# Performance work log

Hardware: AMD Instinct MI355X
Metric: run time of the kernel (lower is better)

Reference implementation:

```python
import jax, jax.numpy as jnp
import numpy as np

HEADS = 16
DIM_HEAD = 64

def setup_inputs() -> dict:
    key = jax.random.key(0)
    ks = jax.random.split(key, 5)
    B, S, D = 2, 2048, 1024
    return {
        "hidden_states": jax.random.normal(ks[0], (B, S, D), dtype=jnp.float32),
        "Wq": jax.random.normal(ks[1], (D, D), dtype=jnp.float32) * (D ** -0.5),
        "Wkv": jax.random.normal(ks[2], (D, D), dtype=jnp.float32) * (D ** -0.5),
        "Wout": jax.random.normal(ks[3], (D, D), dtype=jnp.float32) * (D ** -0.5),
        "bout": jnp.zeros((D,), dtype=jnp.float32),
    }

def reference(hidden_states, Wq, Wkv, Wout, bout):
    B, S, D = hidden_states.shape
    H, Dh = HEADS, DIM_HEAD
    # projections (torch Linear: x @ W.T; here weights are stored as [in, out])
    q = hidden_states @ Wq            # [B, S, D]
    kv = hidden_states @ Wkv          # key == value share the to_kv projection
    q = q.reshape(B, S, H, Dh).transpose(0, 2, 1, 3)   # [B, H, S, Dh]
    k = kv.reshape(B, S, H, Dh).transpose(0, 2, 1, 3)
    v = k
    scale = 1.0 / np.sqrt(Dh).astype(np.float32)
    # ReLU attention: no softmax
    attn = jax.nn.relu(jnp.einsum("bhsd,bhtd->bhst", q, k) * scale)  # [B,H,S,S]
    out = jnp.einsum("bhst,bhtd->bhsd", attn, v)                     # [B,H,S,Dh]
    out = out.transpose(0, 2, 1, 3).reshape(B, S, H * Dh)
    return out @ Wout + bout
```

## Files before the change

### kernel.cpp

```cpp
#include <hip/hip_runtime.h>
#include <hip/hip_bf16.h>

#define HEADS  16
#define DIMH   64
#define NBATCH 2
#define SEQ    2048
#define DMODEL 1024
#define MROWS  (NBATCH * SEQ)

typedef __attribute__((ext_vector_type(8)))  short bf16x8;
typedef __attribute__((ext_vector_type(4)))  float f32x4;
typedef __attribute__((ext_vector_type(16))) float f32x16;
typedef __attribute__((ext_vector_type(4)))  float float4v;
typedef __attribute__((ext_vector_type(4)))  short short4v;

__device__ inline void glds16(const void* g, void* l) {
    __builtin_amdgcn_global_load_lds(
        (const __attribute__((address_space(1))) unsigned int*)g,
        (__attribute__((address_space(3))) unsigned int*)l, 16, 0, 0);
}

#define WAIT_VMCNT(N) asm volatile("s_waitcnt vmcnt(" #N ")" ::: "memory")
#define BARRIER() do { __builtin_amdgcn_s_barrier(); asm volatile("" ::: "memory"); } while (0)

__global__ void cvt_kernel(const float* __restrict__ in,
                           __hip_bfloat16* __restrict__ out, int n4) {
    int i = blockIdx.x * blockDim.x + threadIdx.x;
    if (i >= n4) return;
    float4v v = reinterpret_cast<const float4v*>(in)[i];
    union { short4v s; __hip_bfloat16 h[4]; } u;
#pragma unroll
    for (int j = 0; j < 4; ++j) u.h[j] = __float2bfloat16(v[j]);
    reinterpret_cast<short4v*>(out)[i] = u.s;
}

__global__ void tr_kernel(const float* __restrict__ W,
                          __hip_bfloat16* __restrict__ WT) {
    __shared__ float tile[32][33];
    int i = blockIdx.y * 32 + threadIdx.y;
    int o = blockIdx.x * 32 + threadIdx.x;
    tile[threadIdx.y][threadIdx.x] = W[i * DMODEL + o];
    __syncthreads();
    int oo = blockIdx.x * 32 + threadIdx.y;
    int ii = blockIdx.y * 32 + threadIdx.x;
    WT[oo * DMODEL + ii] = __float2bfloat16(tile[threadIdx.x][threadIdx.y]);
}


__launch_bounds__(512, 4)
__global__ void proj_kernel(const __hip_bfloat16* __restrict__ hsb,
                            const __hip_bfloat16* __restrict__ WqT,
                            const __hip_bfloat16* __restrict__ WkvT,
                            __hip_bfloat16* __restrict__ qb,
                            __hip_bfloat16* __restrict__ kb,
                            __hip_bfloat16* __restrict__ vtb) {
    __shared__ __align__(16) char SLDS[49152];
    char (*Alds)[8192] = (char (*)[8192])SLDS;
    char (*Blds)[8192] = (char (*)[8192])(SLDS + 24576);
    char* CT = SLDS;

    const int tid  = threadIdx.x;
    const int wave = tid >> 6;
    const int lane = tid & 63;
    const int lr = lane & 15;
    const int lk = lane >> 4;
    const int wm = wave >> 1, wn = wave & 1;

    int bid = blockIdx.x;
    bid = (bid & 7) * 64 + (bid >> 3);
    const int xt = bid & 15;
    const int mt = bid >> 4;
    const bool is_q = xt < 8;
    const int mbase = mt * 128;
    const int nbase = (xt & 7) * 128;
    const __hip_bfloat16* __restrict__ WT = is_q ? WqT : WkvT;

    const char* __restrict__ Ab = (const char*)(hsb + (size_t)mbase * DMODEL);
    const char* __restrict__ Bb = (const char*)(WT + (size_t)nbase * DMODEL);

    auto stage = [&](int buf, int k0) {
        const size_t colb = (size_t)k0 * 2 + lk * 16;
        const size_t rowoff = (size_t)(wave * 16 + lr) * (DMODEL * 2);
        glds16(Ab + rowoff + colb, &Alds[buf][wave * 1024]);
        glds16(Bb + rowoff + colb, &Blds[buf][wave * 1024]);
    };

    stage(0, 0);
    stage(1, 32);

    f32x4 acc[2][4] = {};
    int c0 = 0;
    for (int t = 0; t < DMODEL / 32; ++t) {
        if (t < DMODEL / 32 - 1) WAIT_VMCNT(2); else WAIT_VMCNT(0);
        BARRIER();
        if (t + 2 < DMODEL / 32) {
            int sb = c0 + 2; if (sb >= 3) sb -= 3;
            stage(sb, (t + 2) * 32);
        }
        bf16x8 af[2], bfr[4];
#pragma unroll
        for (int i = 0; i < 2; ++i)
            af[i] = *reinterpret_cast<const bf16x8*>(&Alds[c0][(wm * 2 + i) * 1024 + lane * 16]);
#pragma unroll
        for (int j = 0; j < 4; ++j)
            bfr[j] = *reinterpret_cast<const bf16x8*>(&Blds[c0][(wn * 4 + j) * 1024 + lane * 16]);
#pragma unroll
        for (int i = 0; i < 2; ++i)
#pragma unroll
            for (int j = 0; j < 4; ++j)
                acc[i][j] = __builtin_amdgcn_mfma_f32_16x16x32_bf16(af[i], bfr[j], acc[i][j], 0, 0, 0);
        c0 = (c0 + 1 == 3) ? 0 : c0 + 1;
    }

    const float qscale = is_q ? 0.125f : 1.0f;
    const int b_ = mbase >> 11;
    const int s0 = mbase & (SEQ - 1);
    const int h0 = nbase >> 6;
    BARRIER();

#pragma unroll
    for (int i = 0; i < 2; ++i)
#pragma unroll
        for (int j = 0; j < 4; ++j)
#pragma unroll
            for (int r = 0; r < 4; ++r) {
                int m = wm * 32 + i * 16 + lk * 4 + r;
                int n = wn * 64 + j * 16 + lr;
                *reinterpret_cast<__hip_bfloat16*>(
                    &CT[m * 256 + ((n * 2) ^ (((m >> 2) & 7) << 4))]) =
                    __float2bfloat16(acc[i][j][r] * qscale);
            }
    BARRIER();

    __hip_bfloat16* __restrict__ dst0 = is_q ? qb : kb;
#pragma unroll
    for (int p = 0; p < 4; ++p) {
        int g = p * 64 + (tid >> 3);
        int m = g >> 1, hseg = g & 1, o = tid & 7;
        int key = ((m >> 2) & 7) << 4;
        bf16x8 val = *reinterpret_cast<const bf16x8*>(
            &CT[m * 256 + ((hseg * 128 + o * 16) ^ key)]);
        *reinterpret_cast<bf16x8*>(
            &dst0[(((size_t)b_ * HEADS + h0 + hseg) * SEQ + s0 + m) * DIMH + o * 8]) = val;
    }

    if (!is_q) {
        BARRIER();
#pragma unroll
        for (int i = 0; i < 2; ++i)
#pragma unroll
            for (int j = 0; j < 4; ++j)
#pragma unroll
                for (int r = 0; r < 4; ++r) {
                    int m = wm * 32 + i * 16 + lk * 4 + r;
                    int n = wn * 64 + j * 16 + lr;
                    *reinterpret_cast<__hip_bfloat16*>(
                        &CT[n * 256 + ((m * 2) ^ ((n & 7) << 4))]) =
                        __float2bfloat16(acc[i][j][r]);
                }
        BARRIER();
#pragma unroll
        for (int p = 0; p < 4; ++p) {
            int g = p * 64 + (tid >> 3);
            int n = g >> 1, half = g & 1, o = tid & 7;
            int key2 = (n & 7) << 4;
            int D = half * 64 + o * 8;
            int mm = D >> 4, H = o & 1;
            union { unsigned long long d[2]; bf16x8 v; } val;
            val.d[0] = *reinterpret_cast<const unsigned long long*>(
                &CT[n * 256 + ((mm * 32 + H * 8) ^ key2)]);
            val.d[1] = *reinterpret_cast<const unsigned long long*>(
                &CT[n * 256 + ((mm * 32 + 16 + H * 8) ^ key2)]);
            int h = h0 + (n >> 6);
            int dh = n & 63;
            *reinterpret_cast<bf16x8*>(
                &vtb[(((size_t)b_ * HEADS + h) * DIMH + dh) * SEQ + s0 + D]) = val.v;
        }
    }
}

__launch_bounds__(512, 2)
__global__ void outproj_kernel(const __hip_bfloat16* __restrict__ ao,
                               const __hip_bfloat16* __restrict__ WoT,
                               const float* __restrict__ bout,
                               float* __restrict__ out) {
    __shared__ __align__(16) char Alds[3][8192];
    __shared__ __align__(16) char Blds[3][8192];
    const int tid  = threadIdx.x;
    const int wave = tid >> 6;
    const int lane = tid & 63;
    const int lr = lane & 15;
    const int lk = lane >> 4;
    const int wm = wave >> 1, wn = wave & 1;

    int bid = blockIdx.x;
    bid = (bid & 7) * 32 + (bid >> 3);
    const int xt = bid & 7;
    const int mt = bid >> 3;
    const int mbase = mt * 128;
    const int nbase = xt * 128;

    const char* __restrict__ Ab = (const char*)(ao + (size_t)mbase * DMODEL);
    const char* __restrict__ Bb = (const char*)(WoT + (size_t)nbase * DMODEL);

    auto stage = [&](int buf, int k0) {
        const size_t colb = (size_t)k0 * 2 + lk * 16;
        glds16(Ab + (size_t)(wave * 16 + lr) * (DMODEL * 2) + colb,
               &Alds[buf][wave * 1024]);
        glds16(Bb + (size_t)(wave * 16 + lr) * (DMODEL * 2) + colb,
               &Blds[buf][wave * 1024]);
    };

    stage(0, 0);
    stage(1, 32);

    f32x4 acc[2][4] = {};
    int c0 = 0;
    for (int t = 0; t < DMODEL / 32; ++t) {
        if (t < DMODEL / 32 - 1) WAIT_VMCNT(2); else WAIT_VMCNT(0);
        BARRIER();
        if (t + 2 < DMODEL / 32) {
            int sb = c0 + 2; if (sb >= 3) sb -= 3;
            stage(sb, (t + 2) * 32);
        }
        bf16x8 af[2], bfr[4];
#pragma unroll
        for (int i = 0; i < 2; ++i)
            af[i] = *reinterpret_cast<const bf16x8*>(&Alds[c0][(wm * 2 + i) * 1024 + lane * 16]);
#pragma unroll
        for (int j = 0; j < 4; ++j)
            bfr[j] = *reinterpret_cast<const bf16x8*>(&Blds[c0][(wn * 4 + j) * 1024 + lane * 16]);
#pragma unroll
        for (int i = 0; i < 2; ++i)
#pragma unroll
            for (int j = 0; j < 4; ++j)
                acc[i][j] = __builtin_amdgcn_mfma_f32_16x16x32_bf16(af[i], bfr[j], acc[i][j], 0, 0, 0);
        c0 = (c0 + 1 == 3) ? 0 : c0 + 1;
    }

#pragma unroll
    for (int j = 0; j < 4; ++j) {
        const int n = nbase + wn * 64 + j * 16 + lr;
        const float bias = bout[n];
#pragma unroll
        for (int i = 0; i < 2; ++i) {
#pragma unroll
            for (int r = 0; r < 4; ++r) {
                int m = mbase + wm * 32 + i * 16 + lk * 4 + r;
                out[(size_t)m * DMODEL + n] = acc[i][j][r] + bias;
            }
        }
    }
}

__launch_bounds__(512, 2)
__global__ void attn_kernel(const __hip_bfloat16* __restrict__ qb,
                            const __hip_bfloat16* __restrict__ kb,
                            const __hip_bfloat16* __restrict__ vtb,
                            __hip_bfloat16* __restrict__ ao) {
    __shared__ __align__(16) char Klds[4][8192];
    __shared__ __align__(16) char Vlds[4][8192];
    const int lane = threadIdx.x & 63;
    const int wave = threadIdx.x >> 6;
    const int l32  = lane & 31;
    const int hi   = lane >> 5;

    int bid = blockIdx.x;
    bid = (bid & 7) * 32 + (bid >> 3);
    const int qblk = bid & 7;
    const int bh   = bid >> 3;
    const int b_ = bh >> 4, h = bh & 15;
    const int qbase = qblk * 256 + wave * 32;

    const __hip_bfloat16* __restrict__ Q = qb + (size_t)bh * SEQ * DIMH;
    const char* __restrict__ Kg = (const char*)(kb  + (size_t)bh * SEQ * DIMH);
    const char* __restrict__ Vg = (const char*)(vtb + (size_t)bh * DIMH * SEQ);

    bf16x8 qf[4];
#pragma unroll
    for (int ks = 0; ks < 4; ++ks)
        qf[ks] = *reinterpret_cast<const bf16x8*>(
            &Q[(size_t)(qbase + l32) * DIMH + ks * 16 + hi * 8]);

    auto stage = [&](int buf, int t0) {
        glds16(Kg + (size_t)(t0 + (wave >> 2) * 32 + (lane & 31)) * 128 +
                   (wave & 3) * 32 + (lane >> 5) * 16,
               &Klds[buf][wave * 1024]);
        glds16(Vg + (size_t)((wave & 1) * 32 + (lane & 31)) * (SEQ * 2) +
                   (size_t)(t0 + (wave >> 1) * 16) * 2 + (lane >> 5) * 16,
               &Vlds[buf][wave * 1024]);
    };

    f32x16 acco[2] = {};

    auto compute = [&](const char* Kc, const char* Vc) {
        f32x16 sp0 = {}, sp1 = {};
        __builtin_amdgcn_s_setprio(1);
#pragma unroll
        for (int ks = 0; ks < 4; ++ks) {
            bf16x8 k0f = *reinterpret_cast<const bf16x8*>(Kc + ks * 1024 + lane * 16);
            bf16x8 k1f = *reinterpret_cast<const bf16x8*>(Kc + (4 + ks) * 1024 + lane * 16);
            sp0 = __builtin_amdgcn_mfma_f32_32x32x16_bf16(k0f, qf[ks], sp0, 0, 0, 0);
            sp1 = __builtin_amdgcn_mfma_f32_32x32x16_bf16(k1f, qf[ks], sp1, 0, 0, 0);
        }
#pragma unroll
        for (int kt = 0; kt < 4; ++kt) {
            union { __hip_bfloat16 hh[8]; bf16x8 v; } pa;
            const int rb = (kt & 1) * 8;
#pragma unroll
            for (int j = 0; j < 8; ++j) {
                float x = (kt < 2) ? sp0[rb + j] : sp1[rb + j];
                pa.hh[j] = __float2bfloat16(fmaxf(x, 0.f));
            }
#pragma unroll
            for (int nt = 0; nt < 2; ++nt) {
                bf16x8 vbv = *reinterpret_cast<const bf16x8*>(
                    Vc + (kt * 2 + nt) * 1024 + lane * 16);
                acco[nt] = __builtin_amdgcn_mfma_f32_32x32x16_bf16(pa.v, vbv, acco[nt], 0, 0, 0);
            }
        }
        __builtin_amdgcn_s_setprio(0);
    };

    const int NT = SEQ / 64;
    stage(0, 0);
    stage(1, 64);

    for (int t = 0; t < NT; ++t) {
        if (t < NT - 1) WAIT_VMCNT(2); else WAIT_VMCNT(0);
        BARRIER();
        if (t + 2 < NT) stage((t + 2) & 3, (t + 2) * 64);
        compute(Klds[t & 3], Vlds[t & 3]);
    }

#pragma unroll
    for (int nt = 0; nt < 2; ++nt)
#pragma unroll
        for (int r = 0; r < 16; ++r) {
            int q = qbase + (r & 3) + 8 * (r >> 2) + 4 * hi;
            ao[(size_t)(b_ * SEQ + q) * DMODEL + h * 64 + nt * 32 + l32] =
                __float2bfloat16(acco[nt][r]);
        }
}

extern "C" void kernel_launch(void* const* d_in, const int* in_sizes, int n_in,
                              void* d_out, int out_size, void* d_ws, size_t ws_size,
                              hipStream_t stream) {
    const float* hs   = (const float*)d_in[0];
    const float* Wq   = (const float*)d_in[1];
    const float* Wkv  = (const float*)d_in[2];
    const float* Wout = (const float*)d_in[3];
    const float* bout = (const float*)d_in[4];
    float* out = (float*)d_out;

    char* ws = (char*)d_ws;
    size_t off = 0;
    auto alloc = [&](size_t bytes) { char* p = ws + off; off += bytes; return p; };
    __hip_bfloat16* hsb  = (__hip_bfloat16*)alloc((size_t)MROWS * DMODEL * 2);
    __hip_bfloat16* WqT  = (__hip_bfloat16*)alloc((size_t)DMODEL * DMODEL * 2);
    __hip_bfloat16* WkvT = (__hip_bfloat16*)alloc((size_t)DMODEL * DMODEL * 2);
    __hip_bfloat16* WoT  = (__hip_bfloat16*)alloc((size_t)DMODEL * DMODEL * 2);
    __hip_bfloat16* qb   = (__hip_bfloat16*)alloc((size_t)MROWS * DMODEL * 2);
    __hip_bfloat16* kb   = (__hip_bfloat16*)alloc((size_t)MROWS * DMODEL * 2);
    __hip_bfloat16* vtb  = (__hip_bfloat16*)alloc((size_t)MROWS * DMODEL * 2);
    __hip_bfloat16* ao   = hsb;

    cvt_kernel<<<(MROWS * DMODEL / 4 + 255) / 256, 256, 0, stream>>>(hs, hsb, MROWS * DMODEL / 4);
    dim3 trg(32, 32), trb(32, 32);
    tr_kernel<<<trg, trb, 0, stream>>>(Wq, WqT);
    tr_kernel<<<trg, trb, 0, stream>>>(Wkv, WkvT);
    tr_kernel<<<trg, trb, 0, stream>>>(Wout, WoT);

    proj_kernel<<<512, 512, 0, stream>>>(hsb, WqT, WkvT, qb, kb, vtb);

    attn_kernel<<<256, 512, 0, stream>>>(qb, kb, vtb, ao);

    outproj_kernel<<<256, 512, 0, stream>>>(ao, WoT, bout, out);
}
```

Baseline: 126.5 us.

## Split attention over key halves with doubled query tile per wave, fuse prep kernels

The attention kernel now gives each wave 64 query rows instead of 32, so each K/V tile loaded into LDS feeds twice as many MFMAs. To keep the grid at 256 blocks, the key sequence is split into two halves, each block writes fp32 partial outputs, and a new combine kernel sums the two halves and converts to bf16. Separately, the input conversion and the three weight transposes are merged into a single prep launch that uses 64x64 tiles. In exchange, the change adds 32 MB of fp32 partial-output traffic and an extra kernel launch, and raises register pressure in the attention kernel.

```diff
diff --git a/kernel.cpp b/kernel.cpp
--- a/kernel.cpp
+++ b/kernel.cpp
@@ -23,29 +23,59 @@
 #define WAIT_VMCNT(N) asm volatile("s_waitcnt vmcnt(" #N ")" ::: "memory")
 #define BARRIER() do { __builtin_amdgcn_s_barrier(); asm volatile("" ::: "memory"); } while (0)
 
-__global__ void cvt_kernel(const float* __restrict__ in,
-                           __hip_bfloat16* __restrict__ out, int n4) {
+__global__ void prep_kernel(const float* __restrict__ hs,
+                            const float* __restrict__ Wq,
+                            const float* __restrict__ Wkv,
+                            const float* __restrict__ Wout,
+                            __hip_bfloat16* __restrict__ hsb,
+                            __hip_bfloat16* __restrict__ WqT,
+                            __hip_bfloat16* __restrict__ WkvT,
+                            __hip_bfloat16* __restrict__ WoT) {
+    __shared__ float tile[64][65];
+    const int tid = threadIdx.x;
+    const int bid = blockIdx.x;
+    if (bid < 768) {
+        const int w = bid >> 8;
+        const int tnum = bid & 255;
+        const int bx = tnum & 15;
+        const int by = tnum >> 4;
+        const float* __restrict__ W = (w == 0) ? Wq : (w == 1) ? Wkv : Wout;
+        __hip_bfloat16* __restrict__ WT = (w == 0) ? WqT : (w == 1) ? WkvT : WoT;
+        const int ty = tid >> 6, tx = tid & 63;
+#pragma unroll
+        for (int r = 0; r < 16; ++r)
+            tile[ty * 16 + r][tx] = W[(size_t)(by * 64 + ty * 16 + r) * DMODEL + bx * 64 + tx];
+        __syncthreads();
+#pragma unroll
+        for (int r = 0; r < 16; ++r)
+            WT[(size_t)(bx * 64 + ty * 16 + r) * DMODEL + by * 64 + tx] =
+                __float2bfloat16(tile[tx][ty * 16 + r]);
+    } else {
+        const int cb = bid - 768;
+#pragma unroll
+        for (int jj = 0; jj < 4; ++jj) {
+            int i = cb * 1024 + jj * 256 + tid;
+            float4v v = reinterpret_cast<const float4v*>(hs)[i];
+            union { short4v s; __hip_bfloat16 h[4]; } u;
+#pragma unroll
+            for (int j = 0; j < 4; ++j) u.h[j] = __float2bfloat16(v[j]);
+            reinterpret_cast<short4v*>(hsb)[i] = u.s;
+        }
+    }
+}
+
+__global__ void combine_kernel(const float* __restrict__ p0,
+                               const float* __restrict__ p1,
+                               __hip_bfloat16* __restrict__ out, int n4) {
     int i = blockIdx.x * blockDim.x + threadIdx.x;
     if (i >= n4) return;
-    float4v v = reinterpret_cast<const float4v*>(in)[i];
+    float4v a = reinterpret_cast<const float4v*>(p0)[i];
+    float4v b = reinterpret_cast<const float4v*>(p1)[i];
     union { short4v s; __hip_bfloat16 h[4]; } u;
 #pragma unroll
-    for (int j = 0; j < 4; ++j) u.h[j] = __float2bfloat16(v[j]);
+    for (int j = 0; j < 4; ++j) u.h[j] = __float2bfloat16(a[j] + b[j]);
     reinterpret_cast<short4v*>(out)[i] = u.s;
 }
-
-__global__ void tr_kernel(const float* __restrict__ W,
-                          __hip_bfloat16* __restrict__ WT) {
-    __shared__ float tile[32][33];
-    int i = blockIdx.y * 32 + threadIdx.y;
-    int o = blockIdx.x * 32 + threadIdx.x;
-    tile[threadIdx.y][threadIdx.x] = W[i * DMODEL + o];
-    __syncthreads();
-    int oo = blockIdx.x * 32 + threadIdx.y;
-    int ii = blockIdx.y * 32 + threadIdx.x;
-    WT[oo * DMODEL + ii] = __float2bfloat16(tile[threadIdx.x][threadIdx.y]);
-}
-
 
 __launch_bounds__(512, 4)
 __global__ void proj_kernel(const __hip_bfloat16* __restrict__ hsb,
@@ -257,7 +287,7 @@
 __global__ void attn_kernel(const __hip_bfloat16* __restrict__ qb,
                             const __hip_bfloat16* __restrict__ kb,
                             const __hip_bfloat16* __restrict__ vtb,
-                            __hip_bfloat16* __restrict__ ao) {
+                            float* __restrict__ po) {
     __shared__ __align__(16) char Klds[4][8192];
     __shared__ __align__(16) char Vlds[4][8192];
     const int lane = threadIdx.x & 63;
@@ -267,20 +297,24 @@
 
     int bid = blockIdx.x;
     bid = (bid & 7) * 32 + (bid >> 3);
-    const int qblk = bid & 7;
+    const int ts   = bid & 1;
+    const int qblk = (bid >> 1) & 3;
     const int bh   = bid >> 3;
     const int b_ = bh >> 4, h = bh & 15;
-    const int qbase = qblk * 256 + wave * 32;
+    const int qbase = qblk * 512 + wave * 64;
+    const int tbeg = ts * (SEQ / 2);
 
     const __hip_bfloat16* __restrict__ Q = qb + (size_t)bh * SEQ * DIMH;
     const char* __restrict__ Kg = (const char*)(kb  + (size_t)bh * SEQ * DIMH);
     const char* __restrict__ Vg = (const char*)(vtb + (size_t)bh * DIMH * SEQ);
 
-    bf16x8 qf[4];
-#pragma unroll
-    for (int ks = 0; ks < 4; ++ks)
-        qf[ks] = *reinterpret_cast<const bf16x8*>(
-            &Q[(size_t)(qbase + l32) * DIMH + ks * 16 + hi * 8]);
+    bf16x8 qf[2][4];
+#pragma unroll
+    for (int g = 0; g < 2; ++g)
+#pragma unroll
+        for (int ks = 0; ks < 4; ++ks)
+            qf[g][ks] = *reinterpret_cast<const bf16x8*>(
+                &Q[(size_t)(qbase + g * 32 + l32) * DIMH + ks * 16 + hi * 8]);
 
     auto stage = [&](int buf, int t0) {
         glds16(Kg + (size_t)(t0 + (wave >> 2) * 32 + (lane & 31)) * 128 +
@@ -291,56 +325,61 @@
                &Vlds[buf][wave * 1024]);
     };
 
-    f32x16 acco[2] = {};
+    f32x16 acco[2][2] = {};
 
     auto compute = [&](const char* Kc, const char* Vc) {
-        f32x16 sp0 = {}, sp1 = {};
+        f32x16 sp[2][2] = {};
         __builtin_amdgcn_s_setprio(1);
 #pragma unroll
         for (int ks = 0; ks < 4; ++ks) {
             bf16x8 k0f = *reinterpret_cast<const bf16x8*>(Kc + ks * 1024 + lane * 16);
             bf16x8 k1f = *reinterpret_cast<const bf16x8*>(Kc + (4 + ks) * 1024 + lane * 16);
-            sp0 = __builtin_amdgcn_mfma_f32_32x32x16_bf16(k0f, qf[ks], sp0, 0, 0, 0);
-            sp1 = __builtin_amdgcn_mfma_f32_32x32x16_bf16(k1f, qf[ks], sp1, 0, 0, 0);
+            sp[0][0] = __builtin_amdgcn_mfma_f32_32x32x16_bf16(k0f, qf[0][ks], sp[0][0], 0, 0, 0);
+            sp[0][1] = __builtin_amdgcn_mfma_f32_32x32x16_bf16(k1f, qf[0][ks], sp[0][1], 0, 0, 0);
+            sp[1][0] = __builtin_amdgcn_mfma_f32_32x32x16_bf16(k0f, qf[1][ks], sp[1][0], 0, 0, 0);
+            sp[1][1] = __builtin_amdgcn_mfma_f32_32x32x16_bf16(k1f, qf[1][ks], sp[1][1], 0, 0, 0);
         }
 #pragma unroll
         for (int kt = 0; kt < 4; ++kt) {
-            union { __hip_bfloat16 hh[8]; bf16x8 v; } pa;
+            bf16x8 v0 = *reinterpret_cast<const bf16x8*>(Vc + (kt * 2 + 0) * 1024 + lane * 16);
+            bf16x8 v1 = *reinterpret_cast<const bf16x8*>(Vc + (kt * 2 + 1) * 1024 + lane * 16);
             const int rb = (kt & 1) * 8;
 #pragma unroll
-            for (int j = 0; j < 8; ++j) {
-                float x = (kt < 2) ? sp0[rb + j] : sp1[rb + j];
-                pa.hh[j] = __float2bfloat16(fmaxf(x, 0.f));
-            }
-#pragma unroll
-            for (int nt = 0; nt < 2; ++nt) {
-                bf16x8 vbv = *reinterpret_cast<const bf16x8*>(
-                    Vc + (kt * 2 + nt) * 1024 + lane * 16);
-                acco[nt] = __builtin_amdgcn_mfma_f32_32x32x16_bf16(pa.v, vbv, acco[nt], 0, 0, 0);
+            for (int g = 0; g < 2; ++g) {
+                union { __hip_bfloat16 hh[8]; bf16x8 v; } pa;
+#pragma unroll
+                for (int j = 0; j < 8; ++j) {
+                    float x = (kt < 2) ? sp[g][0][rb + j] : sp[g][1][rb + j];
+                    pa.hh[j] = __float2bfloat16(fmaxf(x, 0.f));
+                }
+                acco[g][0] = __builtin_amdgcn_mfma_f32_32x32x16_bf16(pa.v, v0, acco[g][0], 0, 0, 0);
+                acco[g][1] = __builtin_amdgcn_mfma_f32_32x32x16_bf16(pa.v, v1, acco[g][1], 0, 0, 0);
             }
         }
         __builtin_amdgcn_s_setprio(0);
     };
 
-    const int NT = SEQ / 64;
-    stage(0, 0);
-    stage(1, 64);
+    const int NT = SEQ / 2 / 64;
+    stage(0, tbeg);
+    stage(1, tbeg + 64);
 
     for (int t = 0; t < NT; ++t) {
         if (t < NT - 1) WAIT_VMCNT(2); else WAIT_VMCNT(0);
         BARRIER();
-        if (t + 2 < NT) stage((t + 2) & 3, (t + 2) * 64);
+        if (t + 2 < NT) stage((t + 2) & 3, tbeg + (t + 2) * 64);
         compute(Klds[t & 3], Vlds[t & 3]);
     }
 
-#pragma unroll
-    for (int nt = 0; nt < 2; ++nt)
-#pragma unroll
-        for (int r = 0; r < 16; ++r) {
-            int q = qbase + (r & 3) + 8 * (r >> 2) + 4 * hi;
-            ao[(size_t)(b_ * SEQ + q) * DMODEL + h * 64 + nt * 32 + l32] =
-                __float2bfloat16(acco[nt][r]);
-        }
+    float* __restrict__ PO = po + (size_t)ts * MROWS * DMODEL;
+#pragma unroll
+    for (int g = 0; g < 2; ++g)
+#pragma unroll
+        for (int nt = 0; nt < 2; ++nt)
+#pragma unroll
+            for (int r = 0; r < 16; ++r) {
+                int q = qbase + g * 32 + (r & 3) + 8 * (r >> 2) + 4 * hi;
+                PO[(size_t)(b_ * SEQ + q) * DMODEL + h * 64 + nt * 32 + l32] = acco[g][nt][r];
+            }
 }
 
 extern "C" void kernel_launch(void* const* d_in, const int* in_sizes, int n_in,
@@ -363,17 +402,17 @@
     __hip_bfloat16* qb   = (__hip_bfloat16*)alloc((size_t)MROWS * DMODEL * 2);
     __hip_bfloat16* kb   = (__hip_bfloat16*)alloc((size_t)MROWS * DMODEL * 2);
     __hip_bfloat16* vtb  = (__hip_bfloat16*)alloc((size_t)MROWS * DMODEL * 2);
+    float*          po   = (float*)alloc((size_t)2 * MROWS * DMODEL * 4);
     __hip_bfloat16* ao   = hsb;
 
-    cvt_kernel<<<(MROWS * DMODEL / 4 + 255) / 256, 256, 0, stream>>>(hs, hsb, MROWS * DMODEL / 4);
-    dim3 trg(32, 32), trb(32, 32);
-    tr_kernel<<<trg, trb, 0, stream>>>(Wq, WqT);
-    tr_kernel<<<trg, trb, 0, stream>>>(Wkv, WkvT);
-    tr_kernel<<<trg, trb, 0, stream>>>(Wout, WoT);
+    prep_kernel<<<1792, 256, 0, stream>>>(hs, Wq, Wkv, Wout, hsb, WqT, WkvT, WoT);
 
     proj_kernel<<<512, 512, 0, stream>>>(hsb, WqT, WkvT, qb, kb, vtb);
 
-    attn_kernel<<<256, 512, 0, stream>>>(qb, kb, vtb, ao);
+    attn_kernel<<<256, 512, 0, stream>>>(qb, kb, vtb, po);
+
+    combine_kernel<<<(MROWS * DMODEL / 4 + 255) / 256, 256, 0, stream>>>(
+        po, po + (size_t)MROWS * DMODEL, ao, MROWS * DMODEL / 4);
 
     outproj_kernel<<<256, 512, 0, stream>>>(ao, WoT, bout, out);
 }
```

Measured after the change: 118.4 us. -6.4%, faster.
